# Performance work log

Hardware: AMD Instinct MI355X
Metric: run time of the kernel (lower is better)

## Reference

```python
import jax, jax.numpy as jnp
import numpy as np

EPS = 1e-8

def _fft_unit_proj(x):
    # Project each vector to unit magnitude in the Fourier domain (norm_kv=True).
    f = jnp.fft.fft(x, axis=-1)
    return jnp.real(jnp.fft.ifft(f / (jnp.abs(f) + EPS), axis=-1))

def _hrr_key_value_query(k, v, q, causal=True):
    # k, v, q: [B, S, D]
    k = _fft_unit_proj(k)
    v = _fft_unit_proj(v)
    # bind: circular convolution of key and value
    kv = jnp.real(jnp.fft.ifft(jnp.fft.fft(k, axis=-1) * jnp.fft.fft(v, axis=-1), axis=-1))
    # causal associative memory: running sum of bound pairs along sequence
    if causal:
        mem = jnp.cumsum(kv, axis=1)
    else:
        mem = jnp.broadcast_to(jnp.sum(kv, axis=1, keepdims=True), kv.shape)
    # unbind: circular correlation of memory with query
    out = jnp.real(jnp.fft.ifft(jnp.conj(jnp.fft.fft(q, axis=-1)) * jnp.fft.fft(mem, axis=-1), axis=-1))
    return out


def setup_inputs() -> dict:
    key = jax.random.key(0)
    ks = jax.random.split(key, 8)
    B, S, D = 2, 4096, 2048
    sc = 1.0 / np.sqrt(D).astype(np.float32)
    return {
        "hidden_states": jax.random.normal(ks[0], (B, S, D), jnp.float32),
        "base_output": jax.random.normal(ks[1], (B, S, D), jnp.float32),
        "Wq": jax.random.normal(ks[2], (D, D), jnp.float32) * sc,
        "bq": jnp.zeros((D,), jnp.float32),
        "Wk": jax.random.normal(ks[3], (D, D), jnp.float32) * sc,
        "bk": jnp.zeros((D,), jnp.float32),
        "Wv": jax.random.normal(ks[4], (D, D), jnp.float32) * sc,
        "bv": jnp.zeros((D,), jnp.float32),
        "gate": jax.random.normal(ks[5], (1,), jnp.float32) * 0.1,
    }


def reference(hidden_states, base_output, Wq, bq, Wk, bk, Wv, bv, gate):
    # Adapter q/k/v projections (nn.Linear uses y = x @ W.T + b)
    q = jnp.einsum('bsd,ed->bse', hidden_states, Wq) + bq
    k = jnp.einsum('bsd,ed->bse', hidden_states, Wk) + bk
    v = jnp.einsum('bsd,ed->bse', hidden_states, Wv) + bv
    adapter = _hrr_key_value_query(k, v, q, causal=True)
    return base_output + gate * adapter
```

## Files before the change

### kernel.cpp

```cpp
#include <hip/hip_runtime.h>
#include <math.h>

constexpr int D_DIM  = 2048;
constexpr int HALF_D = 1024;
constexpr int B_DIM  = 2;
constexpr int S_DIM  = 4096;
constexpr int NROW   = B_DIM * S_DIM;
constexpr int NCHUNK = 64;
constexpr int CHLEN  = S_DIM / NCHUNK;
constexpr float EPS_ = 1e-8f;

typedef __attribute__((ext_vector_type(8))) short  short8;
typedef __attribute__((ext_vector_type(8))) unsigned short ushort8;
typedef __attribute__((ext_vector_type(4))) float  f32x4;

__device__ __forceinline__ float2 mkf2(float x, float y){ float2 r; r.x=x; r.y=y; return r; }
__device__ __forceinline__ float2 cmulf(float2 a, float2 b){
  return mkf2(fmaf(a.x, b.x, -a.y*b.y), fmaf(a.x, b.y, a.y*b.x));
}
__device__ __forceinline__ unsigned short f2bf(float x){
  unsigned u = __float_as_uint(x);
  u += 0x7fff + ((u >> 16) & 1);
  return (unsigned short)(u >> 16);
}
__device__ __forceinline__ float bf2f(unsigned short h){
  return __uint_as_float(((unsigned)h) << 16);
}

__global__ __launch_bounds__(256)
void cvt_f32_bf16(const float* __restrict__ in, unsigned short* __restrict__ out, int n8)
{
  int i = blockIdx.x * 256 + threadIdx.x;
  if (i >= n8) return;
  const float4* p = (const float4*)in + (size_t)i * 2;
  float4 a = p[0], b = p[1];
  ushort8 o;
  o[0]=f2bf(a.x); o[1]=f2bf(a.y); o[2]=f2bf(a.z); o[3]=f2bf(a.w);
  o[4]=f2bf(b.x); o[5]=f2bf(b.y); o[6]=f2bf(b.z); o[7]=f2bf(b.w);
  *(ushort8*)(out + (size_t)i * 8) = o;
}

__global__ __launch_bounds__(256, 2)
void gemm_fused(const unsigned short* __restrict__ A,
                const unsigned short* __restrict__ Wc,
                const float* __restrict__ bq, const float* __restrict__ bk,
                const float* __restrict__ bv,
                unsigned short* __restrict__ qb, unsigned short* __restrict__ kvb)
{
  constexpr int K = 2048, NT = K / 32;
  __shared__ unsigned short lds[36864];
  const int tid  = threadIdx.x;
  const int wid  = tid >> 6, lane = tid & 63;
  const int wr   = wid >> 1, wc = wid & 1;

  int bid = blockIdx.x;
  int sw  = (bid & 7) * 192 + (bid >> 3);
  const int bm = (sw / 48) * 256, bn = (sw % 48) * 128;

  const int srow = tid >> 2;
  const int skc  = ((tid & 3) ^ ((tid >> 3) & 3)) * 8;
  const unsigned short* Ag = A  + (size_t)(bm + srow) * K + skc;
  const unsigned short* Bg = Wc + (size_t)(bn + srow) * K + skc;

  unsigned short* Abase = lds;
  unsigned short* Bbase = lds + 24576;
  const int stoff = wid * 512;

  const int fr  = lane & 15;
  const int sig = ((lane >> 4) ^ ((lane >> 1) & 3)) * 8;
  const int aro = (wr * 128 + fr) * 32 + sig;
  const int bro = (wc * 64 + fr) * 32 + sig;

  auto stA = [&](int kt, int b, int r) {
    __builtin_amdgcn_global_load_lds(
      (const __attribute__((address_space(1))) void*)(Ag + (size_t)r * 64 * K + kt * 32),
      (__attribute__((address_space(3))) void*)(Abase + b * 8192 + r * 2048 + stoff),
      16, 0, 0);
  };
  auto stB = [&](int kt, int b, int r) {
    __builtin_amdgcn_global_load_lds(
      (const __attribute__((address_space(1))) void*)(Bg + (size_t)r * 64 * K + kt * 32),
      (__attribute__((address_space(3))) void*)(Bbase + b * 4096 + r * 2048 + stoff),
      16, 0, 0);
  };

  f32x4 acc[8][4];
#pragma unroll
  for (int i = 0; i < 8; ++i)
#pragma unroll
    for (int j = 0; j < 4; ++j) acc[i][j] = (f32x4){0.f, 0.f, 0.f, 0.f};

  stA(0, 0, 0); stA(0, 0, 1); stA(0, 0, 2); stA(0, 0, 3); stB(0, 0, 0); stB(0, 0, 1);
  stA(1, 1, 0); stA(1, 1, 1); stA(1, 1, 2); stA(1, 1, 3); stB(1, 1, 0); stB(1, 1, 1);
  asm volatile("s_waitcnt vmcnt(6)" ::: "memory");
  __builtin_amdgcn_s_barrier();
  __builtin_amdgcn_sched_barrier(0);

  int c = 0;
#pragma unroll 1
  for (int kt = 0; kt < NT; ++kt) {
    const unsigned short* Ab = Abase + c * 8192;
    const unsigned short* Bb = Bbase + c * 4096;
    int nb = c + 2; if (nb >= 3) nb -= 3;
    const bool st = (kt < NT - 2);

    if (st) { stA(kt + 2, nb, 0); stA(kt + 2, nb, 1); stA(kt + 2, nb, 2); stA(kt + 2, nb, 3); }
    short8 af0[4], bfr[4];
#pragma unroll
    for (int i = 0; i < 4; ++i) af0[i] = *(const short8*)(Ab + aro + i * 512);
#pragma unroll
    for (int j = 0; j < 4; ++j) bfr[j] = *(const short8*)(Bb + bro + j * 512);
    __builtin_amdgcn_s_barrier();
    asm volatile("s_waitcnt lgkmcnt(0)" ::: "memory");
    __builtin_amdgcn_sched_barrier(0);
    __builtin_amdgcn_s_setprio(1);
#pragma unroll
    for (int i = 0; i < 4; ++i)
#pragma unroll
      for (int j = 0; j < 4; ++j)
        acc[i][j] = __builtin_amdgcn_mfma_f32_16x16x32_bf16(af0[i], bfr[j], acc[i][j], 0, 0, 0);
    __builtin_amdgcn_s_setprio(0);
    __builtin_amdgcn_s_barrier();

    if (st) { stB(kt + 2, nb, 0); stB(kt + 2, nb, 1); }
    short8 af1[4];
#pragma unroll
    for (int i = 0; i < 4; ++i) af1[i] = *(const short8*)(Ab + aro + 2048 + i * 512);
    __builtin_amdgcn_s_barrier();
    asm volatile("s_waitcnt lgkmcnt(0)" ::: "memory");
    __builtin_amdgcn_sched_barrier(0);
    __builtin_amdgcn_s_setprio(1);
#pragma unroll
    for (int i = 0; i < 4; ++i)
#pragma unroll
      for (int j = 0; j < 4; ++j)
        acc[4 + i][j] = __builtin_amdgcn_mfma_f32_16x16x32_bf16(af1[i], bfr[j], acc[4 + i][j], 0, 0, 0);
    __builtin_amdgcn_s_setprio(0);
    if (st)                 asm volatile("s_waitcnt vmcnt(6)" ::: "memory");
    else if (kt == NT - 2)  asm volatile("s_waitcnt vmcnt(0)" ::: "memory");
    __builtin_amdgcn_s_barrier();
    c = (c == 2) ? 0 : c + 1;
  }

  const int seg = bn >> 11;
  const float* bp = (seg == 0) ? bq : (seg == 1) ? bk : bv;
  float bias_j[4];
#pragma unroll
  for (int j = 0; j < 4; ++j)
    bias_j[j] = bp[(bn + wc * 64 + j * 16 + fr) & 2047];
  const int er = (lane >> 4) * 4;
  unsigned short* dst = (seg == 0) ? qb : kvb;
  const size_t rstride = (seg == 0) ? 2048 : 4096;
  const int coff = (seg == 2) ? 2048 : 0;
#pragma unroll
  for (int I = 0; I < 8; ++I) {
    int row = bm + wr * 128 + I * 16 + er;
#pragma unroll
    for (int j = 0; j < 4; ++j) {
      int col = (bn + wc * 64 + j * 16 + fr) & 2047;
#pragma unroll
      for (int r = 0; r < 4; ++r) {
        float val = acc[I][j][r] + bias_j[j];
        dst[(size_t)(row + r) * rstride + coff + col] = f2bf(val);
      }
    }
  }
}

__device__ __forceinline__ int XS(int i){ return i ^ (((i >> 5) ^ (i >> 10)) & 31); }
__device__ __forceinline__ int TS(int i){ return i ^ ((i >> 5) & 31); }

__device__ __forceinline__ float2 mulmi(float2 w){ return mkf2(w.y, -w.x); }
__device__ __forceinline__ float2 mulw8(float2 w){
  const float c = 0.70710678118654752f;
  return mkf2(c * (w.x + w.y), c * (w.y - w.x));
}
__device__ __forceinline__ void bfly(float2& a, float2& b, float2 w){
  float2 v = cmulf(w, b);
  b = mkf2(a.x - v.x, a.y - v.y);
  a = mkf2(a.x + v.x, a.y + v.y);
}
__device__ __forceinline__ void bflyc(float2& a, float2& b, float2 w){
  float2 d = mkf2(a.x - b.x, a.y - b.y);
  a = mkf2(a.x + b.x, a.y + b.y);
  b = mkf2(fmaf(d.x, w.x, d.y * w.y), fmaf(d.y, w.x, -d.x * w.y));
}

__device__ __forceinline__ void fwd8(float2 e[8], float2 wA, float2 wB0, float2 wC0){
  bfly(e[0], e[1], wA); bfly(e[2], e[3], wA); bfly(e[4], e[5], wA); bfly(e[6], e[7], wA);
  float2 wB1 = mulmi(wB0);
  bfly(e[0], e[2], wB0); bfly(e[1], e[3], wB1); bfly(e[4], e[6], wB0); bfly(e[5], e[7], wB1);
  float2 wC1 = mulw8(wC0), wC2 = mulmi(wC0), wC3 = mulmi(wC1);
  bfly(e[0], e[4], wC0); bfly(e[1], e[5], wC1); bfly(e[2], e[6], wC2); bfly(e[3], e[7], wC3);
}
__device__ __forceinline__ void inv8(float2 e[8], float2 wA, float2 wB0, float2 wC0){
  float2 wC1 = mulw8(wC0), wC2 = mulmi(wC0), wC3 = mulmi(wC1);
  bflyc(e[0], e[4], wC0); bflyc(e[1], e[5], wC1); bflyc(e[2], e[6], wC2); bflyc(e[3], e[7], wC3);
  float2 wB1 = mulmi(wB0);
  bflyc(e[0], e[2], wB0); bflyc(e[1], e[3], wB1); bflyc(e[4], e[6], wB0); bflyc(e[5], e[7], wB1);
  bflyc(e[0], e[1], wA); bflyc(e[2], e[3], wA); bflyc(e[4], e[5], wA); bflyc(e[6], e[7], wA);
}

__device__ __forceinline__ float2 twld(const float* twr, const float* twi, int i){
  int s = TS(i);
  return mkf2(twr[s], twi[s]);
}

__device__ void fft_fwd(float2* X, const float* twr, const float* twi, int t)
{
  const float2 one = mkf2(1.f, 0.f);
  {
    int b = 8 * t;
    float2 e[8];
#pragma unroll
    for (int r = 0; r < 8; ++r) e[r] = X[XS(b + r)];
    fwd8(e, one, one, one);
#pragma unroll
    for (int r = 0; r < 8; ++r) X[XS(b + r)] = e[r];
  }
  __syncthreads();
  {
    int u = t >> 5, b = 64 * (t & 31) + u;
    float2 e[8];
#pragma unroll
    for (int r = 0; r < 8; ++r) e[r] = X[XS(b + 8 * r)];
    fwd8(e, twld(twr,twi,128*u), twld(twr,twi,64*u), twld(twr,twi,32*u));
#pragma unroll
    for (int r = 0; r < 8; ++r) X[XS(b + 8 * r)] = e[r];
  }
  __syncthreads();
  {
    int u = t & 63, b = 512 * (t >> 6) + u;
    float2 e[8];
#pragma unroll
    for (int r = 0; r < 8; ++r) e[r] = X[XS(b + 64 * r)];
    fwd8(e, twld(twr,twi,16*u), twld(twr,twi,8*u), twld(twr,twi,4*u));
#pragma unroll
    for (int r = 0; r < 8; ++r) X[XS(b + 64 * r)] = e[r];
  }
  __syncthreads();
#pragma unroll
  for (int h = 0; h < 2; ++h) {
    int u = t + 256 * h;
    float2 f[4];
#pragma unroll
    for (int r = 0; r < 4; ++r) f[r] = X[XS(u + 512 * r)];
    float2 wA = twld(twr,twi,2*u), wB0 = twld(twr,twi,u), wB1 = mulmi(wB0);
    bfly(f[0], f[1], wA);  bfly(f[2], f[3], wA);
    bfly(f[0], f[2], wB0); bfly(f[1], f[3], wB1);
#pragma unroll
    for (int r = 0; r < 4; ++r) X[XS(u + 512 * r)] = f[r];
  }
  __syncthreads();
}

__device__ void fft_inv(float2* X, const float* twr, const float* twi, int t)
{
  const float2 one = mkf2(1.f, 0.f);
#pragma unroll
  for (int h = 0; h < 2; ++h) {
    int u = t + 256 * h;
    float2 f[4];
#pragma unroll
    for (int r = 0; r < 4; ++r) f[r] = X[XS(u + 512 * r)];
    float2 wA = twld(twr,twi,2*u), wB0 = twld(twr,twi,u), wB1 = mulmi(wB0);
    bflyc(f[0], f[2], wB0); bflyc(f[1], f[3], wB1);
    bflyc(f[0], f[1], wA);  bflyc(f[2], f[3], wA);
#pragma unroll
    for (int r = 0; r < 4; ++r) X[XS(u + 512 * r)] = f[r];
  }
  __syncthreads();
  {
    int u = t & 63, b = 512 * (t >> 6) + u;
    float2 e[8];
#pragma unroll
    for (int r = 0; r < 8; ++r) e[r] = X[XS(b + 64 * r)];
    inv8(e, twld(twr,twi,16*u), twld(twr,twi,8*u), twld(twr,twi,4*u));
#pragma unroll
    for (int r = 0; r < 8; ++r) X[XS(b + 64 * r)] = e[r];
  }
  __syncthreads();
  {
    int u = t >> 5, b = 64 * (t & 31) + u;
    float2 e[8];
#pragma unroll
    for (int r = 0; r < 8; ++r) e[r] = X[XS(b + 8 * r)];
    inv8(e, twld(twr,twi,128*u), twld(twr,twi,64*u), twld(twr,twi,32*u));
#pragma unroll
    for (int r = 0; r < 8; ++r) X[XS(b + 8 * r)] = e[r];
  }
  __syncthreads();
  {
    int b = 8 * t;
    float2 e[8];
#pragma unroll
    for (int r = 0; r < 8; ++r) e[r] = X[XS(b + r)];
    inv8(e, one, one, one);
#pragma unroll
    for (int r = 0; r < 8; ++r) X[XS(b + r)] = e[r];
  }
  __syncthreads();
}

__global__ __launch_bounds__(256)
void twiddle_init(float2* __restrict__ twg)
{
  int i = blockIdx.x * 256 + threadIdx.x;
  if (i < HALF_D) {
    float sv, cv;
    sincosf(-6.283185307179586f * (float)i / (float)D_DIM, &sv, &cv);
    twg[i] = mkf2(cv, sv);
  }
}

__global__ __launch_bounds__(256)
void fftkv_kernel(unsigned short* __restrict__ kvb, const float2* __restrict__ twg)
{
  __shared__ float2 X[D_DIM];
  __shared__ float twr[HALF_D], twi[HALF_D];
  const int t = threadIdx.x;
  const size_t row = blockIdx.x;
  const unsigned short* kvrow = kvb + row * 4096;

  for (int i = t; i < HALF_D; i += 256) {
    float2 w = twg[i]; int s = TS(i); twr[s] = w.x; twi[s] = w.y;
  }
  {
    int i0 = t * 8;
    ushort8 k8 = *(const ushort8*)(kvrow + i0);
    ushort8 v8 = *(const ushort8*)(kvrow + 2048 + i0);
#pragma unroll
    for (int r = 0; r < 8; ++r) {
      int i = i0 + r;
      int p = __brev((unsigned)i) >> 21;
      X[XS(p)] = mkf2(bf2f(k8[r]), bf2f(v8[r]));
    }
  }
  __syncthreads();
  fft_fwd(X, twr, twi, t);

  unsigned int* outp = (unsigned int*)(kvb + row * 4096);
  for (int d = t; d < HALF_D; d += 256) {
    float2 p;
    if (d == 0) {
      float2 z0 = X[XS(0)], zn = X[XS(HALF_D)];
      float k0 = z0.x, v0 = z0.y, kn = zn.x, vn = zn.y;
      float p0 = (k0 / (fabsf(k0) + EPS_)) * (v0 / (fabsf(v0) + EPS_));
      float pn = (kn / (fabsf(kn) + EPS_)) * (vn / (fabsf(vn) + EPS_));
      p = mkf2(p0, pn);
    } else {
      float2 A = X[XS(d)];
      float2 Bc = X[XS(D_DIM - d)];
      float2 Bj = mkf2(Bc.x, -Bc.y);
      float2 Fk = mkf2(0.5f * (A.x + Bj.x), 0.5f * (A.y + Bj.y));
      float2 tt = mkf2(0.5f * (A.x - Bj.x), 0.5f * (A.y - Bj.y));
      float2 Fv = mkf2(tt.y, -tt.x);
      float sa = 1.f / (sqrtf(Fk.x*Fk.x + Fk.y*Fk.y) + EPS_);
      float sb = 1.f / (sqrtf(Fv.x*Fv.x + Fv.y*Fv.y) + EPS_);
      p = cmulf(Fk, Fv);
      float sc = sa * sb;
      p.x *= sc; p.y *= sc;
    }
    outp[d] = (unsigned)f2bf(p.x) | ((unsigned)f2bf(p.y) << 16);
  }
}

__global__ __launch_bounds__(256)
void scan_partial(const unsigned short* __restrict__ kvb, float2* __restrict__ part)
{
  int gid = blockIdx.x * 256 + threadIdx.x;
  int q4 = gid & 255;
  int chunk = (gid >> 8) & (NCHUNK - 1);
  int b = gid >> 14;
  const unsigned short* p = kvb + (size_t)(b * S_DIM + chunk * CHLEN) * 4096 + q4 * 8;
  float ar[4] = {0,0,0,0}, ai[4] = {0,0,0,0};
  for (int s = 0; s < CHLEN; ++s) {
    ushort8 v = *(const ushort8*)(p + (size_t)s * 4096);
#pragma unroll
    for (int e = 0; e < 4; ++e) { ar[e] += bf2f(v[2*e]); ai[e] += bf2f(v[2*e+1]); }
  }
  float2* pp = part + (size_t)(b * NCHUNK + chunk) * HALF_D + q4 * 4;
#pragma unroll
  for (int e = 0; e < 4; ++e) pp[e] = mkf2(ar[e], ai[e]);
}

__global__ __launch_bounds__(256)
void scan_offsets(float2* __restrict__ part)
{
  int gid = blockIdx.x * 256 + threadIdx.x;
  int d = gid & (HALF_D - 1);
  int b = gid >> 10;
  float2* p = part + (size_t)b * (NCHUNK * HALF_D) + d;
  float2 acc = mkf2(0.f, 0.f);
  for (int c = 0; c < NCHUNK; ++c) {
    float2 v = p[(size_t)c * HALF_D];
    p[(size_t)c * HALF_D] = acc;
    acc.x += v.x; acc.y += v.y;
  }
}

__global__ __launch_bounds__(256)
void scan_apply(unsigned short* __restrict__ kvb, const float2* __restrict__ part)
{
  int gid = blockIdx.x * 256 + threadIdx.x;
  int q4 = gid & 255;
  int chunk = (gid >> 8) & (NCHUNK - 1);
  int b = gid >> 14;
  unsigned short* p = kvb + (size_t)(b * S_DIM + chunk * CHLEN) * 4096 + q4 * 8;
  const float2* pp = part + (size_t)(b * NCHUNK + chunk) * HALF_D + q4 * 4;
  float ar[4], ai[4];
#pragma unroll
  for (int e = 0; e < 4; ++e) { float2 v = pp[e]; ar[e] = v.x; ai[e] = v.y; }
  for (int s = 0; s < CHLEN; ++s) {
    ushort8 v = *(const ushort8*)(p + (size_t)s * 4096);
    ushort8 o;
#pragma unroll
    for (int e = 0; e < 4; ++e) {
      ar[e] += bf2f(v[2*e]); ai[e] += bf2f(v[2*e+1]);
      o[2*e] = f2bf(ar[e]); o[2*e+1] = f2bf(ai[e]);
    }
    *(ushort8*)(p + (size_t)s * 4096) = o;
  }
}

__global__ __launch_bounds__(256)
void final_kernel(const unsigned short* __restrict__ qb,
                  const unsigned short* __restrict__ kvb,
                  const float* __restrict__ base, const float* __restrict__ gate,
                  const float2* __restrict__ twg, float* __restrict__ out)
{
  __shared__ float2 X[D_DIM];
  __shared__ float twr[HALF_D], twi[HALF_D];
  const int t = threadIdx.x;
  const size_t row = blockIdx.x;
  const unsigned short* qrow = qb + row * 2048;
  const unsigned short* mrow = kvb + row * 4096;

  for (int i = t; i < HALF_D; i += 256) {
    float2 w = twg[i]; int s = TS(i); twr[s] = w.x; twi[s] = w.y;
  }
  {
    int i0 = t * 8;
    ushort8 q8 = *(const ushort8*)(qrow + i0);
#pragma unroll
    for (int r = 0; r < 8; ++r) {
      int i = i0 + r;
      int p = __brev((unsigned)i) >> 21;
      X[XS(p)] = mkf2(bf2f(q8[r]), 0.f);
    }
  }
  __syncthreads();
  fft_fwd(X, twr, twi, t);

  for (int d = t; d < HALF_D; d += 256) {
    float fmre = bf2f(mrow[2*d]), fmim = bf2f(mrow[2*d+1]);
    if (d == 0) {
      float2 f0 = X[XS(0)], f1 = X[XS(HALF_D)];
      X[XS(0)]      = mkf2(f0.x * fmre, -f0.y * fmre);
      X[XS(HALF_D)] = mkf2(f1.x * fmim, -f1.y * fmim);
    } else {
      float2 fq = X[XS(d)];
      X[XS(d)] = mkf2(fq.x*fmre + fq.y*fmim, fq.x*fmim - fq.y*fmre);
      float2 f2 = X[XS(D_DIM - d)];
      X[XS(D_DIM - d)] = mkf2(f2.x*fmre - f2.y*fmim, -f2.x*fmim - f2.y*fmre);
    }
  }
  __syncthreads();
  fft_inv(X, twr, twi, t);

  const float gv = gate[0] * (1.f / (float)D_DIM);
  const float* brow = base + row * D_DIM;
  float* orow = out + row * D_DIM;
  for (int i = t; i < D_DIM; i += 256) {
    int p = __brev((unsigned)i) >> 21;
    orow[i] = brow[i] + gv * X[XS(p)].x;
  }
}

extern "C" void kernel_launch(void* const* d_in, const int* in_sizes, int n_in,
                              void* d_out, int out_size, void* d_ws, size_t ws_size,
                              hipStream_t stream)
{
  const float* hs   = (const float*)d_in[0];
  const float* base = (const float*)d_in[1];
  const float* Wq   = (const float*)d_in[2];
  const float* bq   = (const float*)d_in[3];
  const float* Wk   = (const float*)d_in[4];
  const float* bk   = (const float*)d_in[5];
  const float* Wv   = (const float*)d_in[6];
  const float* bv   = (const float*)d_in[7];
  const float* gate = (const float*)d_in[8];
  float* out  = (float*)d_out;

  char* ws = (char*)d_ws;
  unsigned short* hsb = (unsigned short*)ws;
  unsigned short* wqb = (unsigned short*)(ws + 33554432);
  unsigned short* wkb = wqb + (size_t)D_DIM * D_DIM;
  unsigned short* wvb = wkb + (size_t)D_DIM * D_DIM;
  unsigned short* kvb = (unsigned short*)(ws + 58720256);
  unsigned short* qb  = (unsigned short*)(ws + 58720256 + 67108864);
  float2* part = (float2*)(ws + 58720256 + 67108864 + 33554432);
  float2* twg  = (float2*)ws;

  {
    int n8 = (NROW * D_DIM) / 8;
    cvt_f32_bf16<<<n8 / 256, 256, 0, stream>>>(hs, hsb, n8);
    int w8 = (D_DIM * D_DIM) / 8;
    cvt_f32_bf16<<<w8 / 256, 256, 0, stream>>>(Wq, wqb, w8);
    cvt_f32_bf16<<<w8 / 256, 256, 0, stream>>>(Wk, wkb, w8);
    cvt_f32_bf16<<<w8 / 256, 256, 0, stream>>>(Wv, wvb, w8);
  }

  gemm_fused<<<1536, 256, 0, stream>>>(hsb, wqb, bq, bk, bv, qb, kvb);

  twiddle_init<<<4, 256, 0, stream>>>(twg);

  fftkv_kernel<<<NROW, 256, 0, stream>>>(kvb, twg);

  scan_partial<<<128, 256, 0, stream>>>(kvb, part);
  scan_offsets<<<(B_DIM * HALF_D) / 256, 256, 0, stream>>>(part);
  scan_apply<<<128, 256, 0, stream>>>(kvb, part);

  final_kernel<<<NROW, 256, 0, stream>>>(qb, kvb, base, gate, twg, out);
}
```

Before: 404.4 us.

## Retile QKV GEMM to 256x256 blocks with 8 waves and 8-phase pipeline

Rewrites the fused bf16 QKV projection GEMM to use 512-thread blocks computing 256x256 output tiles with K-steps of 64. It uses a double-buffered LDS layout with an XOR swizzle and an eight-phase loop that interleaves global-to-LDS loads with MFMA groups. The larger tile improves operand reuse per LDS byte and halves the block count. In exchange it raises LDS use to 128KB per block and adds register pressure, which may limit occupancy.

```diff
diff --git a/kernel.cpp b/kernel.cpp
--- a/kernel.cpp
+++ b/kernel.cpp
@@ -40,106 +40,122 @@
   *(ushort8*)(out + (size_t)i * 8) = o;
 }
 
-__global__ __launch_bounds__(256, 2)
+__global__ __launch_bounds__(512, 2)
 void gemm_fused(const unsigned short* __restrict__ A,
                 const unsigned short* __restrict__ Wc,
                 const float* __restrict__ bq, const float* __restrict__ bk,
                 const float* __restrict__ bv,
                 unsigned short* __restrict__ qb, unsigned short* __restrict__ kvb)
 {
-  constexpr int K = 2048, NT = K / 32;
-  __shared__ unsigned short lds[36864];
+  constexpr int K = 2048, NITER = 16;
+  __shared__ unsigned short lds[65536];
   const int tid  = threadIdx.x;
   const int wid  = tid >> 6, lane = tid & 63;
-  const int wr   = wid >> 1, wc = wid & 1;
+  const int wr   = wid >> 2, wc = wid & 3;
 
   int bid = blockIdx.x;
-  int sw  = (bid & 7) * 192 + (bid >> 3);
-  const int bm = (sw / 48) * 256, bn = (sw % 48) * 128;
-
-  const int srow = tid >> 2;
-  const int skc  = ((tid & 3) ^ ((tid >> 3) & 3)) * 8;
+  int sw  = (bid & 7) * 96 + (bid >> 3);
+  const int bm = (sw / 24) * 256, bn = (sw % 24) * 256;
+
+  const int srow = tid >> 3;
+  const int skc  = ((tid & 7) ^ (srow & 7)) * 8;
   const unsigned short* Ag = A  + (size_t)(bm + srow) * K + skc;
   const unsigned short* Bg = Wc + (size_t)(bn + srow) * K + skc;
-
-  unsigned short* Abase = lds;
-  unsigned short* Bbase = lds + 24576;
+  unsigned short* Al = lds;
+  unsigned short* Bl = lds + 32768;
   const int stoff = wid * 512;
 
-  const int fr  = lane & 15;
-  const int sig = ((lane >> 4) ^ ((lane >> 1) & 3)) * 8;
-  const int aro = (wr * 128 + fr) * 32 + sig;
-  const int bro = (wc * 64 + fr) * 32 + sig;
-
-  auto stA = [&](int kt, int b, int r) {
+  auto stA = [&](int kt, int d, int h, int r) {
     __builtin_amdgcn_global_load_lds(
-      (const __attribute__((address_space(1))) void*)(Ag + (size_t)r * 64 * K + kt * 32),
-      (__attribute__((address_space(3))) void*)(Abase + b * 8192 + r * 2048 + stoff),
+      (const __attribute__((address_space(1))) void*)(Ag + (size_t)(h * 128 + r * 64) * K + kt * 64),
+      (__attribute__((address_space(3))) void*)(Al + d * 16384 + h * 8192 + r * 4096 + stoff),
       16, 0, 0);
   };
-  auto stB = [&](int kt, int b, int r) {
+  auto stB = [&](int kt, int d, int h, int r) {
     __builtin_amdgcn_global_load_lds(
-      (const __attribute__((address_space(1))) void*)(Bg + (size_t)r * 64 * K + kt * 32),
-      (__attribute__((address_space(3))) void*)(Bbase + b * 4096 + r * 2048 + stoff),
+      (const __attribute__((address_space(1))) void*)(Bg + (size_t)(h * 128 + r * 64) * K + kt * 64),
+      (__attribute__((address_space(3))) void*)(Bl + d * 16384 + h * 8192 + r * 4096 + stoff),
       16, 0, 0);
   };
 
+  const int frow = lane & 15;
+  const int kq   = lane >> 4;
+  int ksw[2];
+  ksw[0] = ((0 * 4 + kq) ^ (frow & 7)) * 8;
+  ksw[1] = ((1 * 4 + kq) ^ (frow & 7)) * 8;
+  const int arow0 = (wr * 128 + frow) * 64;
+  const int brow0 = (wc * 64 + frow) * 64;
+
   f32x4 acc[8][4];
 #pragma unroll
   for (int i = 0; i < 8; ++i)
 #pragma unroll
     for (int j = 0; j < 4; ++j) acc[i][j] = (f32x4){0.f, 0.f, 0.f, 0.f};
 
-  stA(0, 0, 0); stA(0, 0, 1); stA(0, 0, 2); stA(0, 0, 3); stB(0, 0, 0); stB(0, 0, 1);
-  stA(1, 1, 0); stA(1, 1, 1); stA(1, 1, 2); stA(1, 1, 3); stB(1, 1, 0); stB(1, 1, 1);
-  asm volatile("s_waitcnt vmcnt(6)" ::: "memory");
+  stA(0, 0, 0, 0); stA(0, 0, 0, 1); stA(0, 0, 1, 0); stA(0, 0, 1, 1);
+  stB(0, 0, 0, 0); stB(0, 0, 0, 1); stB(0, 0, 1, 0); stB(0, 0, 1, 1);
+  stB(1, 1, 0, 0); stB(1, 1, 0, 1); stB(1, 1, 1, 0); stB(1, 1, 1, 1);
+  asm volatile("s_waitcnt vmcnt(4)" ::: "memory");
   __builtin_amdgcn_s_barrier();
   __builtin_amdgcn_sched_barrier(0);
 
-  int c = 0;
 #pragma unroll 1
-  for (int kt = 0; kt < NT; ++kt) {
-    const unsigned short* Ab = Abase + c * 8192;
-    const unsigned short* Bb = Bbase + c * 4096;
-    int nb = c + 2; if (nb >= 3) nb -= 3;
-    const bool st = (kt < NT - 2);
-
-    if (st) { stA(kt + 2, nb, 0); stA(kt + 2, nb, 1); stA(kt + 2, nb, 2); stA(kt + 2, nb, 3); }
-    short8 af0[4], bfr[4];
-#pragma unroll
-    for (int i = 0; i < 4; ++i) af0[i] = *(const short8*)(Ab + aro + i * 512);
-#pragma unroll
-    for (int j = 0; j < 4; ++j) bfr[j] = *(const short8*)(Bb + bro + j * 512);
-    __builtin_amdgcn_s_barrier();
-    asm volatile("s_waitcnt lgkmcnt(0)" ::: "memory");
-    __builtin_amdgcn_sched_barrier(0);
-    __builtin_amdgcn_s_setprio(1);
-#pragma unroll
-    for (int i = 0; i < 4; ++i)
-#pragma unroll
-      for (int j = 0; j < 4; ++j)
-        acc[i][j] = __builtin_amdgcn_mfma_f32_16x16x32_bf16(af0[i], bfr[j], acc[i][j], 0, 0, 0);
-    __builtin_amdgcn_s_setprio(0);
-    __builtin_amdgcn_s_barrier();
-
-    if (st) { stB(kt + 2, nb, 0); stB(kt + 2, nb, 1); }
-    short8 af1[4];
-#pragma unroll
-    for (int i = 0; i < 4; ++i) af1[i] = *(const short8*)(Ab + aro + 2048 + i * 512);
-    __builtin_amdgcn_s_barrier();
-    asm volatile("s_waitcnt lgkmcnt(0)" ::: "memory");
-    __builtin_amdgcn_sched_barrier(0);
-    __builtin_amdgcn_s_setprio(1);
-#pragma unroll
-    for (int i = 0; i < 4; ++i)
-#pragma unroll
-      for (int j = 0; j < 4; ++j)
-        acc[4 + i][j] = __builtin_amdgcn_mfma_f32_16x16x32_bf16(af1[i], bfr[j], acc[4 + i][j], 0, 0, 0);
-    __builtin_amdgcn_s_setprio(0);
-    if (st)                 asm volatile("s_waitcnt vmcnt(6)" ::: "memory");
-    else if (kt == NT - 2)  asm volatile("s_waitcnt vmcnt(0)" ::: "memory");
-    __builtin_amdgcn_s_barrier();
-    c = (c == 2) ? 0 : c + 1;
+  for (int it = 0; it < NITER; ++it) {
+    const bool nl = (it < NITER - 1);
+    const int t1 = 2 * it + 1;
+    short8 bfr[8];
+#pragma unroll
+    for (int ph = 0; ph < 8; ++ph) {
+      const int g  = ph & 3;
+      const int db = ph >> 2;
+      const unsigned short* Ab = Al + db * 16384;
+      const unsigned short* Bb = Bl + db * 16384;
+
+      if      (ph == 0) { stA(t1, 1, 0, 0); stA(t1, 1, 0, 1); }
+      else if (ph == 1) { stA(t1, 1, 1, 0); stA(t1, 1, 1, 1); }
+      else if (ph == 2) { if (nl) { stB(t1 + 1, 0, 0, 0); stB(t1 + 1, 0, 0, 1); } }
+      else if (ph == 3) { if (nl) { stB(t1 + 1, 0, 1, 0); stB(t1 + 1, 0, 1, 1); } }
+      else if (ph == 4) { if (nl) { stA(t1 + 1, 0, 0, 0); stA(t1 + 1, 0, 0, 1); } }
+      else if (ph == 5) { if (nl) { stA(t1 + 1, 0, 1, 0); stA(t1 + 1, 0, 1, 1); } }
+      else if (ph == 6) { if (nl) { stB(t1 + 2, 1, 0, 0); stB(t1 + 2, 1, 0, 1); } }
+      else              { if (nl) { stB(t1 + 2, 1, 1, 0); stB(t1 + 2, 1, 1, 1); } }
+
+      short8 af[2][2];
+#pragma unroll
+      for (int q = 0; q < 2; ++q)
+#pragma unroll
+        for (int ks = 0; ks < 2; ++ks)
+          af[q][ks] = *(const short8*)(Ab + arow0 + (2 * g + q) * 1024 + ksw[ks]);
+      if (g == 0) {
+#pragma unroll
+        for (int nf = 0; nf < 4; ++nf)
+#pragma unroll
+          for (int ks = 0; ks < 2; ++ks)
+            bfr[nf * 2 + ks] = *(const short8*)(Bb + brow0 + nf * 1024 + ksw[ks]);
+      }
+
+      __builtin_amdgcn_s_barrier();
+      asm volatile("s_waitcnt lgkmcnt(0)" ::: "memory");
+      __builtin_amdgcn_sched_barrier(0);
+      __builtin_amdgcn_s_setprio(1);
+#pragma unroll
+      for (int ks = 0; ks < 2; ++ks)
+#pragma unroll
+        for (int q = 0; q < 2; ++q)
+#pragma unroll
+          for (int nf = 0; nf < 4; ++nf)
+            acc[2 * g + q][nf] = __builtin_amdgcn_mfma_f32_16x16x32_bf16(
+                af[q][ks], bfr[nf * 2 + ks], acc[2 * g + q][nf], 0, 0, 0);
+      __builtin_amdgcn_s_setprio(0);
+
+      if (ph == 3) {
+        if (nl) asm volatile("s_waitcnt vmcnt(4)" ::: "memory");
+        else    asm volatile("s_waitcnt vmcnt(0)" ::: "memory");
+      } else if (ph == 7) {
+        if (nl) asm volatile("s_waitcnt vmcnt(4)" ::: "memory");
+      }
+      __builtin_amdgcn_s_barrier();
+    }
   }
 
   const int seg = bn >> 11;
@@ -147,7 +163,7 @@
   float bias_j[4];
 #pragma unroll
   for (int j = 0; j < 4; ++j)
-    bias_j[j] = bp[(bn + wc * 64 + j * 16 + fr) & 2047];
+    bias_j[j] = bp[(bn + wc * 64 + j * 16 + frow) & 2047];
   const int er = (lane >> 4) * 4;
   unsigned short* dst = (seg == 0) ? qb : kvb;
   const size_t rstride = (seg == 0) ? 2048 : 4096;
@@ -157,7 +173,7 @@
     int row = bm + wr * 128 + I * 16 + er;
 #pragma unroll
     for (int j = 0; j < 4; ++j) {
-      int col = (bn + wc * 64 + j * 16 + fr) & 2047;
+      int col = (bn + wc * 64 + j * 16 + frow) & 2047;
 #pragma unroll
       for (int r = 0; r < 4; ++r) {
         float val = acc[I][j][r] + bias_j[j];
@@ -511,7 +527,7 @@
     cvt_f32_bf16<<<w8 / 256, 256, 0, stream>>>(Wv, wvb, w8);
   }
 
-  gemm_fused<<<1536, 256, 0, stream>>>(hsb, wqb, bq, bk, bv, qb, kvb);
+  gemm_fused<<<768, 512, 0, stream>>>(hsb, wqb, bq, bk, bv, qb, kvb);
 
   twiddle_init<<<4, 256, 0, stream>>>(twg);
 
```

After: 376.4 us. 6.9% less time.
